# Performance work log

Hardware: AMD Instinct MI355X
Metric: run time of the kernel (lower is better)

Reference implementation:

```python
import jax, jax.numpy as jnp
import numpy as np

# MLA config (matches init_kwargs)
D = 2048
D_PRE_HEAD = 128
HEAD_NUM = 16
D_ROPE = D_PRE_HEAD // 2          # 64
DC_V = D_PRE_HEAD                 # 128
DC_KV = 4 * D_PRE_HEAD            # 512
DC_Q = 3 * DC_KV                  # 1536
Q_HEAD_DIM = D_PRE_HEAD + D_ROPE  # 192
MEG_D = D_PRE_HEAD + DC_V         # 256
MAX_LEN = 8192
EPS = 1e-7
BATCH, SEQ = 2, 2048


def rms_norm(x, w):
    x32 = x.astype(jnp.float32)
    var = jnp.mean(x32 * x32, axis=-1, keepdims=True)
    return w * (x32 * jax.lax.rsqrt(var + EPS)).astype(x.dtype)


def rope_reshape(x):
    # de-interleave pairs: [x0,x1,x2,x3,...] -> [x0,x2,...,x1,x3,...]
    b, h, s, d = x.shape
    return x.reshape(b, h, s, d // 2, 2).swapaxes(-1, -2).reshape(b, h, s, d)


def rope_rotate(x):
    half = x.shape[-1] // 2
    return jnp.concatenate([-x[..., half:], x[..., :half]], axis=-1)


def rope_tables(dtype=jnp.float32):
    inv_freq = 1.0 / (10000.0 ** (jnp.arange(0, D_ROPE, 2, dtype=jnp.float32) / D_ROPE))
    t = jnp.arange(MAX_LEN, dtype=jnp.float32)
    freqs = jnp.outer(t, inv_freq)                 # [MAX_LEN, D_ROPE/2]
    emb = jnp.concatenate([freqs, freqs], axis=-1)  # [MAX_LEN, D_ROPE]
    return jnp.cos(emb).astype(dtype), jnp.sin(emb).astype(dtype)


def setup_inputs() -> dict:
    key = jax.random.key(0)
    ks = jax.random.split(key, 8)
    s = 0.02
    x = jax.random.normal(ks[0], (BATCH, SEQ, D), dtype=jnp.float32)
    pos_ids = jnp.broadcast_to(jnp.arange(SEQ, dtype=jnp.int32)[None, :], (BATCH, SEQ))
    return {
        "x": x,
        "pos_ids": pos_ids,
        "w_q_down": jax.random.normal(ks[1], (DC_Q, D), dtype=jnp.float32) * s,
        "q_norm_w": jnp.ones((DC_Q,), dtype=jnp.float32),
        "w_q_up": jax.random.normal(ks[2], (HEAD_NUM * Q_HEAD_DIM, DC_Q), dtype=jnp.float32) * s,
        "w_kv_down": jax.random.normal(ks[3], (DC_KV + D_ROPE, D), dtype=jnp.float32) * s,
        "kv_norm_w": jnp.ones((DC_KV,), dtype=jnp.float32),
        "w_kv_up": jax.random.normal(ks[4], (HEAD_NUM * MEG_D, DC_KV), dtype=jnp.float32) * s,
        "w_out": jax.random.normal(ks[5], (D, HEAD_NUM * DC_V), dtype=jnp.float32) * s,
    }


def reference(x, pos_ids, w_q_down, q_norm_w, w_q_up, w_kv_down, kv_norm_w, w_kv_up, w_out):
    b, s, _ = x.shape
    # --- Q path: low-rank down -> norm -> up ---
    q = rms_norm(x @ w_q_down.T, q_norm_w) @ w_q_up.T          # [b,s,H*q_head_dim]
    q = q.reshape(b, s, HEAD_NUM, Q_HEAD_DIM).transpose(0, 2, 1, 3)  # [b,H,s,qhd]
    q_nope, q_rope = q[..., :D_PRE_HEAD], q[..., D_PRE_HEAD:]
    # --- KV path: shared compressed latent + decoupled rope key ---
    ckv_all = x @ w_kv_down.T                                   # [b,s,dc_kv+d_rope]
    c_kv, k_rope = ckv_all[..., :DC_KV], ckv_all[..., DC_KV:]
    c_kv = rms_norm(c_kv, kv_norm_w)
    kv = (c_kv @ w_kv_up.T).reshape(b, s, HEAD_NUM, MEG_D).transpose(0, 2, 1, 3)
    k_nope, value = kv[..., :D_PRE_HEAD], kv[..., D_PRE_HEAD:]  # [b,H,s,128] each
    k_rope = k_rope.reshape(b, s, 1, D_ROPE).transpose(0, 2, 1, 3)  # [b,1,s,64]
    # --- RoPE (decoupled path) ---
    cos, sin = rope_tables(x.dtype)
    cos_q = cos[pos_ids][:, None]   # [b,1,s,64]
    sin_q = sin[pos_ids][:, None]
    qr = rope_reshape(q_rope)
    kr = rope_reshape(k_rope)
    q_rope = qr * cos_q + rope_rotate(qr) * sin_q
    k_rope = kr * cos_q + rope_rotate(kr) * sin_q
    # --- attention ---
    query = jnp.concatenate([q_nope, q_rope], axis=-1)          # [b,H,s,192]
    key = jnp.concatenate(
        [k_nope, jnp.broadcast_to(k_rope, (b, HEAD_NUM, s, D_ROPE))], axis=-1)
    scale = 1.0 / jnp.sqrt(jnp.asarray(Q_HEAD_DIM, dtype=x.dtype))
    scores = jnp.einsum('bhqd,bhkd->bhqk', query, key) * scale
    causal = jnp.where(jnp.tril(jnp.ones((s, s), dtype=bool)), 0.0, -jnp.inf)
    scores = scores + causal[None, None].astype(scores.dtype)
    probs = jax.nn.softmax(scores, axis=-1)
    attn = jnp.einsum('bhqk,bhkd->bhqd', probs, value)          # [b,H,s,128]
    attn = attn.transpose(0, 2, 1, 3).reshape(b, s, HEAD_NUM * DC_V)
    return attn @ w_out.T
```

## Files before the change

### kernel.cpp

```cpp
#include <hip/hip_runtime.h>
#include <hip/hip_bf16.h>
#include <math.h>


#define T_TOK   4096
#define SEQ_LEN 2048
#define NB      2
#define NHEAD   16
#define DMODEL  2048
#define DCQ     1536
#define DCKV    512
#define DROPE   64
#define QHD     192
#define MEGD    256

typedef unsigned short u16;
typedef unsigned int   u32;
typedef __attribute__((ext_vector_type(8))) short short8v;
typedef __attribute__((ext_vector_type(4))) float f32x4;

__device__ __forceinline__ u16 f2bf(float f) {
    u32 u = __float_as_uint(f);
    u32 r = u + 0x7FFFu + ((u >> 16) & 1u);
    return (u16)(r >> 16);
}
__device__ __forceinline__ float bf2f(u16 h) {
    return __uint_as_float(((u32)h) << 16);
}

__global__ __launch_bounds__(256) void gemm_split_nt(
    const float* __restrict__ A, int lda,
    const float* __restrict__ W, int ldw,
    float* __restrict__ C, int ldc, int K)
{
    __shared__ __align__(16) u16 Ahs[64][32];
    __shared__ __align__(16) u16 Als[64][32];
    __shared__ __align__(16) u16 Whs[64][32];
    __shared__ __align__(16) u16 Wls[64][32];

    const int tid  = threadIdx.x;
    const int wave = tid >> 6;
    const int lane = tid & 63;
    const int wr = (wave >> 1) * 32;
    const int wc = (wave & 1) * 32;
    const int m0 = blockIdx.y * 64;
    const int n0 = blockIdx.x * 64;

    const int srow = tid >> 2;
    const int scol = (tid & 3) * 8;

    f32x4 acc[2][2];
    #pragma unroll
    for (int i = 0; i < 2; ++i)
        #pragma unroll
        for (int j = 0; j < 2; ++j)
            acc[i][j] = (f32x4){0.f, 0.f, 0.f, 0.f};

    const float* Ap = A + (size_t)(m0 + srow) * lda + scol;
    const float* Wp = W + (size_t)(n0 + srow) * ldw + scol;

    const int fr = lane & 15;
    const int kg = (lane >> 4) * 8;

    for (int k0 = 0; k0 < K; k0 += 32) {
        float av[8], wv[8];
        *(float4*)&av[0] = *(const float4*)(Ap + k0);
        *(float4*)&av[4] = *(const float4*)(Ap + k0 + 4);
        *(float4*)&wv[0] = *(const float4*)(Wp + k0);
        *(float4*)&wv[4] = *(const float4*)(Wp + k0 + 4);
        short8v ah, al, wh, wl;
        #pragma unroll
        for (int j = 0; j < 8; ++j) {
            u16 hb = f2bf(av[j]);
            ah[j] = (short)hb;
            al[j] = (short)f2bf(av[j] - bf2f(hb));
            u16 hw = f2bf(wv[j]);
            wh[j] = (short)hw;
            wl[j] = (short)f2bf(wv[j] - bf2f(hw));
        }
        __syncthreads();
        *(short8v*)&Ahs[srow][scol] = ah;
        *(short8v*)&Als[srow][scol] = al;
        *(short8v*)&Whs[srow][scol] = wh;
        *(short8v*)&Wls[srow][scol] = wl;
        __syncthreads();

        short8v afh[2], afl[2], wfh[2], wfl[2];
        #pragma unroll
        for (int i = 0; i < 2; ++i) {
            afh[i] = *(const short8v*)&Ahs[wr + i * 16 + fr][kg];
            afl[i] = *(const short8v*)&Als[wr + i * 16 + fr][kg];
            wfh[i] = *(const short8v*)&Whs[wc + i * 16 + fr][kg];
            wfl[i] = *(const short8v*)&Wls[wc + i * 16 + fr][kg];
        }
        #pragma unroll
        for (int i = 0; i < 2; ++i)
            #pragma unroll
            for (int j = 0; j < 2; ++j) {
                acc[i][j] = __builtin_amdgcn_mfma_f32_16x16x32_bf16(afh[i], wfh[j], acc[i][j], 0, 0, 0);
                acc[i][j] = __builtin_amdgcn_mfma_f32_16x16x32_bf16(afh[i], wfl[j], acc[i][j], 0, 0, 0);
                acc[i][j] = __builtin_amdgcn_mfma_f32_16x16x32_bf16(afl[i], wfh[j], acc[i][j], 0, 0, 0);
            }
    }

    const int rq = (lane >> 4) * 4;
    #pragma unroll
    for (int i = 0; i < 2; ++i)
        #pragma unroll
        for (int j = 0; j < 2; ++j)
            #pragma unroll
            for (int r = 0; r < 4; ++r)
                C[(size_t)(m0 + wr + i * 16 + rq + r) * ldc + (n0 + wc + j * 16 + fr)]
                    = acc[i][j][r];
}

template <int NPT>
__global__ __launch_bounds__(256) void rmsnorm_kernel(
    float* __restrict__ data, int stride, const float* __restrict__ w, int width)
{
    const int row = blockIdx.x;
    float* p = data + (size_t)row * stride;
    const int tid = threadIdx.x;

    float v[NPT];
    float ss = 0.f;
    #pragma unroll
    for (int i = 0; i < NPT; ++i) { v[i] = p[tid + i * 256]; ss += v[i] * v[i]; }
    #pragma unroll
    for (int off = 32; off; off >>= 1) ss += __shfl_xor(ss, off, 64);

    __shared__ float red[4];
    if ((tid & 63) == 0) red[tid >> 6] = ss;
    __syncthreads();
    ss = red[0] + red[1] + red[2] + red[3];

    const float scale = rsqrtf(ss / (float)width + 1e-7f);
    #pragma unroll
    for (int i = 0; i < NPT; ++i)
        p[tid + i * 256] = w[tid + i * 256] * (v[i] * scale);
}

__device__ __forceinline__ void rope_row(const float* __restrict__ vin,
                                         float* __restrict__ vout, float p)
{
    float buf[64];
    #pragma unroll
    for (int j = 0; j < 64; ++j) buf[j] = vin[j];
    #pragma unroll
    for (int j = 0; j < 32; ++j) {
        float f = powf(10000.f, -(float)j * (1.f / 32.f));
        float a = p * f;
        float c = cosf(a), s = sinf(a);
        vout[j]      = buf[2 * j] * c - buf[2 * j + 1] * s;
        vout[32 + j] = buf[2 * j + 1] * c + buf[2 * j] * s;
    }
}

__global__ __launch_bounds__(256) void rope_q_kernel(float* __restrict__ q,
                                                     const int* __restrict__ pos)
{
    const int idx = blockIdx.x * 256 + threadIdx.x;
    if (idx >= T_TOK * NHEAD) return;
    const int t = idx >> 4, h = idx & 15;
    float* v = q + (size_t)t * (NHEAD * QHD) + h * QHD + 128;
    rope_row(v, v, (float)pos[t]);
}

__global__ __launch_bounds__(256) void rope_k_kernel(const float* __restrict__ ckv,
                                                     const int* __restrict__ pos,
                                                     float* __restrict__ kr)
{
    const int t = blockIdx.x * 256 + threadIdx.x;
    if (t >= T_TOK) return;
    rope_row(ckv + (size_t)t * (DCKV + DROPE) + DCKV, kr + (size_t)t * DROPE,
             (float)pos[t]);
}

#define BQA   64
#define BKA   32
#define KSTR2 200
#define VSTR2 40
#define PSTR2 40

__global__ __launch_bounds__(256) void mla_attn_mfma(
    const float* __restrict__ q,
    const float* __restrict__ kv,
    const float* __restrict__ kr,
    float* __restrict__ o)
{
    __shared__ __align__(16) u16 KhS[BKA][KSTR2];
    __shared__ __align__(16) u16 KlS[BKA][KSTR2];
    __shared__ __align__(16) u16 VhS[128][VSTR2];
    __shared__ __align__(16) u16 VlS[128][VSTR2];
    __shared__ __align__(16) u16 PhS[4][16][PSTR2];
    __shared__ __align__(16) u16 PlS[4][16][PSTR2];

    const int qt = (int)(gridDim.x - 1) - (int)blockIdx.x;
    const int h  = blockIdx.y;
    const int b  = blockIdx.z;
    const int q0 = qt * BQA;
    const int tid  = threadIdx.x;
    const int wave = tid >> 6;
    const int lane = tid & 63;
    const int fr = lane & 15;
    const int gp = lane >> 4;
    const int kg = gp * 8;

    short8v qh[6], ql[6];
    {
        const float* qrow = q + (size_t)(b * SEQ_LEN + q0 + wave * 16 + fr) * (NHEAD * QHD)
                              + h * QHD;
        #pragma unroll
        for (int ks = 0; ks < 6; ++ks) {
            float v8[8];
            *(float4*)&v8[0] = *(const float4*)(qrow + ks * 32 + kg);
            *(float4*)&v8[4] = *(const float4*)(qrow + ks * 32 + kg + 4);
            #pragma unroll
            for (int j = 0; j < 8; ++j) {
                u16 hb = f2bf(v8[j]);
                qh[ks][j] = (short)hb;
                ql[ks][j] = (short)f2bf(v8[j] - bf2f(hb));
            }
        }
    }

    f32x4 acc_o[8];
    #pragma unroll
    for (int i = 0; i < 8; ++i) acc_o[i] = (f32x4){0.f, 0.f, 0.f, 0.f};
    float mrow[4] = {-1e30f, -1e30f, -1e30f, -1e30f};
    float lrow[4] = {0.f, 0.f, 0.f, 0.f};

    const float scale = 0.07216878364870323f;
    const int ntile = 2 * qt + 2;
    const int qmax_w = q0 + 16 * wave + 15;

    for (int kt = 0; kt < ntile; ++kt) {
        const int k0 = kt * BKA;
        __syncthreads();

        {
            const int krow = tid >> 3;
            const int c0 = (tid & 7) * 24;
            const int tk = b * SEQ_LEN + k0 + krow;
            float v24[24];
            #pragma unroll
            for (int i = 0; i < 6; ++i) {
                const int d = c0 + i * 4;
                float4 vv = (d < 128)
                    ? *(const float4*)(kv + (size_t)tk * (NHEAD * MEGD) + h * MEGD + d)
                    : *(const float4*)(kr + (size_t)tk * DROPE + (d - 128));
                *(float4*)&v24[i * 4] = vv;
            }
            #pragma unroll
            for (int i = 0; i < 6; ++i) {
                ushort4 hh, ll;
                u16* hp = &hh.x; u16* lp = &ll.x;
                #pragma unroll
                for (int j = 0; j < 4; ++j) {
                    float f = v24[i * 4 + j];
                    u16 hb = f2bf(f);
                    hp[j] = hb;
                    lp[j] = f2bf(f - bf2f(hb));
                }
                *(ushort4*)&KhS[krow][c0 + i * 4] = hh;
                *(ushort4*)&KlS[krow][c0 + i * 4] = ll;
            }
        }
        {
            const int kq = (tid & 7) * 4;
            const int dq = (tid >> 3) * 4;
            float4 vv[4];
            #pragma unroll
            for (int r = 0; r < 4; ++r) {
                const int tk = b * SEQ_LEN + k0 + kq + r;
                vv[r] = *(const float4*)(kv + (size_t)tk * (NHEAD * MEGD) + h * MEGD + 128 + dq);
            }
            const float* vp = (const float*)&vv[0];
            #pragma unroll
            for (int i = 0; i < 4; ++i) {
                ushort4 hh, ll;
                u16* hp = &hh.x; u16* lp = &ll.x;
                #pragma unroll
                for (int r = 0; r < 4; ++r) {
                    float f = vp[r * 4 + i];
                    u16 hb = f2bf(f);
                    hp[r] = hb;
                    lp[r] = f2bf(f - bf2f(hb));
                }
                *(ushort4*)&VhS[dq + i][kq] = hh;
                *(ushort4*)&VlS[dq + i][kq] = ll;
            }
        }
        __syncthreads();

        if (k0 <= qmax_w) {
            f32x4 s0 = (f32x4){0.f, 0.f, 0.f, 0.f};
            f32x4 s1 = (f32x4){0.f, 0.f, 0.f, 0.f};
            #pragma unroll
            for (int ks = 0; ks < 6; ++ks) {
                short8v kh0 = *(const short8v*)&KhS[fr][ks * 32 + kg];
                short8v kl0 = *(const short8v*)&KlS[fr][ks * 32 + kg];
                short8v kh1 = *(const short8v*)&KhS[fr + 16][ks * 32 + kg];
                short8v kl1 = *(const short8v*)&KlS[fr + 16][ks * 32 + kg];
                s0 = __builtin_amdgcn_mfma_f32_16x16x32_bf16(qh[ks], kh0, s0, 0, 0, 0);
                s0 = __builtin_amdgcn_mfma_f32_16x16x32_bf16(qh[ks], kl0, s0, 0, 0, 0);
                s0 = __builtin_amdgcn_mfma_f32_16x16x32_bf16(ql[ks], kh0, s0, 0, 0, 0);
                s1 = __builtin_amdgcn_mfma_f32_16x16x32_bf16(qh[ks], kh1, s1, 0, 0, 0);
                s1 = __builtin_amdgcn_mfma_f32_16x16x32_bf16(qh[ks], kl1, s1, 0, 0, 0);
                s1 = __builtin_amdgcn_mfma_f32_16x16x32_bf16(ql[ks], kh1, s1, 0, 0, 0);
            }
            float alpha[4];
            #pragma unroll
            for (int r = 0; r < 4; ++r) {
                const int qglob = q0 + wave * 16 + 4 * gp + r;
                float sc0 = (k0 + fr      <= qglob) ? s0[r] * scale : -1e30f;
                float sc1 = (k0 + 16 + fr <= qglob) ? s1[r] * scale : -1e30f;
                float mt = fmaxf(sc0, sc1);
                mt = fmaxf(mt, __shfl_xor(mt, 1, 64));
                mt = fmaxf(mt, __shfl_xor(mt, 2, 64));
                mt = fmaxf(mt, __shfl_xor(mt, 4, 64));
                mt = fmaxf(mt, __shfl_xor(mt, 8, 64));
                const float mnew = fmaxf(mrow[r], mt);
                alpha[r] = __expf(mrow[r] - mnew);
                const float p0 = __expf(sc0 - mnew);
                const float p1 = __expf(sc1 - mnew);
                float ps = p0 + p1;
                ps += __shfl_xor(ps, 1, 64);
                ps += __shfl_xor(ps, 2, 64);
                ps += __shfl_xor(ps, 4, 64);
                ps += __shfl_xor(ps, 8, 64);
                lrow[r] = lrow[r] * alpha[r] + ps;
                mrow[r] = mnew;
                u16 h0 = f2bf(p0);
                PhS[wave][4 * gp + r][fr]      = h0;
                PlS[wave][4 * gp + r][fr]      = f2bf(p0 - bf2f(h0));
                u16 h1 = f2bf(p1);
                PhS[wave][4 * gp + r][fr + 16] = h1;
                PlS[wave][4 * gp + r][fr + 16] = f2bf(p1 - bf2f(h1));
            }
            #pragma unroll
            for (int f2 = 0; f2 < 8; ++f2)
                #pragma unroll
                for (int r = 0; r < 4; ++r)
                    acc_o[f2][r] *= alpha[r];
            short8v ph = *(const short8v*)&PhS[wave][fr][kg];
            short8v pl = *(const short8v*)&PlS[wave][fr][kg];
            #pragma unroll
            for (int f2 = 0; f2 < 8; ++f2) {
                short8v vh = *(const short8v*)&VhS[fr + 16 * f2][kg];
                short8v vl = *(const short8v*)&VlS[fr + 16 * f2][kg];
                acc_o[f2] = __builtin_amdgcn_mfma_f32_16x16x32_bf16(ph, vh, acc_o[f2], 0, 0, 0);
                acc_o[f2] = __builtin_amdgcn_mfma_f32_16x16x32_bf16(ph, vl, acc_o[f2], 0, 0, 0);
                acc_o[f2] = __builtin_amdgcn_mfma_f32_16x16x32_bf16(pl, vh, acc_o[f2], 0, 0, 0);
            }
        }
    }

    float inv[4];
    #pragma unroll
    for (int r = 0; r < 4; ++r) inv[r] = 1.f / lrow[r];
    #pragma unroll
    for (int r = 0; r < 4; ++r) {
        const size_t t = (size_t)(b * SEQ_LEN + q0 + wave * 16 + 4 * gp + r);
        float* dst = o + t * (NHEAD * 128) + h * 128 + fr;
        #pragma unroll
        for (int f2 = 0; f2 < 8; ++f2)
            dst[16 * f2] = acc_o[f2][r] * inv[r];
    }
}

extern "C" void kernel_launch(void* const* d_in, const int* in_sizes, int n_in,
                              void* d_out, int out_size, void* d_ws, size_t ws_size,
                              hipStream_t stream)
{
    const float* x         = (const float*)d_in[0];
    const int*   pos       = (const int*)d_in[1];
    const float* w_q_down  = (const float*)d_in[2];
    const float* q_norm_w  = (const float*)d_in[3];
    const float* w_q_up    = (const float*)d_in[4];
    const float* w_kv_down = (const float*)d_in[5];
    const float* kv_norm_w = (const float*)d_in[6];
    const float* w_kv_up   = (const float*)d_in[7];
    const float* w_out     = (const float*)d_in[8];
    float* out = (float*)d_out;

    float* ws = (float*)d_ws;
    float* ao   = ws;
    float* q_dn = ws;
    float* ckv  = ws + (size_t)T_TOK * 2048;
    float* q_up = ckv + (size_t)T_TOK * (DCKV + DROPE);
    float* kvb  = q_up + (size_t)T_TOK * (NHEAD * QHD);
    float* kr   = kvb + (size_t)T_TOK * (NHEAD * MEGD);

    dim3 blk(256);
    gemm_split_nt<<<dim3(DCQ / 64, T_TOK / 64), blk, 0, stream>>>(
        x, DMODEL, w_q_down, DMODEL, q_dn, DCQ, DMODEL);
    gemm_split_nt<<<dim3((DCKV + DROPE) / 64, T_TOK / 64), blk, 0, stream>>>(
        x, DMODEL, w_kv_down, DMODEL, ckv, DCKV + DROPE, DMODEL);
    rmsnorm_kernel<6><<<T_TOK, 256, 0, stream>>>(q_dn, DCQ, q_norm_w, DCQ);
    rmsnorm_kernel<2><<<T_TOK, 256, 0, stream>>>(ckv, DCKV + DROPE, kv_norm_w, DCKV);
    rope_k_kernel<<<T_TOK / 256, 256, 0, stream>>>(ckv, pos, kr);
    gemm_split_nt<<<dim3((NHEAD * QHD) / 64, T_TOK / 64), blk, 0, stream>>>(
        q_dn, DCQ, w_q_up, DCQ, q_up, NHEAD * QHD, DCQ);
    gemm_split_nt<<<dim3((NHEAD * MEGD) / 64, T_TOK / 64), blk, 0, stream>>>(
        ckv, DCKV + DROPE, w_kv_up, DCKV, kvb, NHEAD * MEGD, DCKV);
    rope_q_kernel<<<(T_TOK * NHEAD) / 256, 256, 0, stream>>>(q_up, pos);
    mla_attn_mfma<<<dim3(SEQ_LEN / BQA, NHEAD, NB), dim3(256), 0, stream>>>(
        q_up, kvb, kr, ao);
    gemm_split_nt<<<dim3(DMODEL / 64, T_TOK / 64), blk, 0, stream>>>(
        ao, DMODEL, w_out, DMODEL, out, DMODEL, DMODEL);
}
```

Before: 1.400 ms.

## Enlarge split-bf16 GEMM tiles to 128x128, swizzle attention LDS, precompute RoPE frequencies

```diff
diff --git a/kernel.cpp b/kernel.cpp
--- a/kernel.cpp
+++ b/kernel.cpp
@@ -28,90 +28,99 @@
     return __uint_as_float(((u32)h) << 16);
 }
 
+#define GSTR 40
+
 __global__ __launch_bounds__(256) void gemm_split_nt(
     const float* __restrict__ A, int lda,
     const float* __restrict__ W, int ldw,
-    float* __restrict__ C, int ldc, int K)
-{
-    __shared__ __align__(16) u16 Ahs[64][32];
-    __shared__ __align__(16) u16 Als[64][32];
-    __shared__ __align__(16) u16 Whs[64][32];
-    __shared__ __align__(16) u16 Wls[64][32];
+    float* __restrict__ C, int ldc, int K, int N)
+{
+    __shared__ __align__(16) u16 Ahs[128][GSTR];
+    __shared__ __align__(16) u16 Als[128][GSTR];
+    __shared__ __align__(16) u16 Whs[128][GSTR];
+    __shared__ __align__(16) u16 Wls[128][GSTR];
 
     const int tid  = threadIdx.x;
     const int wave = tid >> 6;
     const int lane = tid & 63;
-    const int wr = (wave >> 1) * 32;
-    const int wc = (wave & 1) * 32;
-    const int m0 = blockIdx.y * 64;
-    const int n0 = blockIdx.x * 64;
-
-    const int srow = tid >> 2;
-    const int scol = (tid & 3) * 8;
-
-    f32x4 acc[2][2];
-    #pragma unroll
-    for (int i = 0; i < 2; ++i)
-        #pragma unroll
-        for (int j = 0; j < 2; ++j)
-            acc[i][j] = (f32x4){0.f, 0.f, 0.f, 0.f};
-
-    const float* Ap = A + (size_t)(m0 + srow) * lda + scol;
-    const float* Wp = W + (size_t)(n0 + srow) * ldw + scol;
-
+    const int wr = (wave >> 1) * 64;
+    const int wc = (wave & 1) * 64;
+    const int m0 = blockIdx.y * 128;
+    const int n0 = blockIdx.x * 128;
     const int fr = lane & 15;
     const int kg = (lane >> 4) * 8;
 
+    f32x4 acc[4][4];
+    #pragma unroll
+    for (int i = 0; i < 4; ++i)
+        #pragma unroll
+        for (int j = 0; j < 4; ++j)
+            acc[i][j] = (f32x4){0.f, 0.f, 0.f, 0.f};
+
+    const int r0 = tid >> 2,          c0 = (tid & 3) * 8;
+    const int r1 = (tid + 256) >> 2,  c1 = c0;
+    const int an0 = m0 + r0, an1 = m0 + r1;
+    const int wn0 = (n0 + r0 < N) ? n0 + r0 : N - 1;
+    const int wn1 = (n0 + r1 < N) ? n0 + r1 : N - 1;
+
     for (int k0 = 0; k0 < K; k0 += 32) {
-        float av[8], wv[8];
-        *(float4*)&av[0] = *(const float4*)(Ap + k0);
-        *(float4*)&av[4] = *(const float4*)(Ap + k0 + 4);
-        *(float4*)&wv[0] = *(const float4*)(Wp + k0);
-        *(float4*)&wv[4] = *(const float4*)(Wp + k0 + 4);
-        short8v ah, al, wh, wl;
+        float a0[8], a1[8], w0[8], w1[8];
+        *(float4*)&a0[0] = *(const float4*)(A + (size_t)an0 * lda + k0 + c0);
+        *(float4*)&a0[4] = *(const float4*)(A + (size_t)an0 * lda + k0 + c0 + 4);
+        *(float4*)&a1[0] = *(const float4*)(A + (size_t)an1 * lda + k0 + c1);
+        *(float4*)&a1[4] = *(const float4*)(A + (size_t)an1 * lda + k0 + c1 + 4);
+        *(float4*)&w0[0] = *(const float4*)(W + (size_t)wn0 * ldw + k0 + c0);
+        *(float4*)&w0[4] = *(const float4*)(W + (size_t)wn0 * ldw + k0 + c0 + 4);
+        *(float4*)&w1[0] = *(const float4*)(W + (size_t)wn1 * ldw + k0 + c1);
+        *(float4*)&w1[4] = *(const float4*)(W + (size_t)wn1 * ldw + k0 + c1 + 4);
+
+        short8v a0h, a0l, a1h, a1l, w0h, w0l, w1h, w1l;
         #pragma unroll
         for (int j = 0; j < 8; ++j) {
-            u16 hb = f2bf(av[j]);
-            ah[j] = (short)hb;
-            al[j] = (short)f2bf(av[j] - bf2f(hb));
-            u16 hw = f2bf(wv[j]);
-            wh[j] = (short)hw;
-            wl[j] = (short)f2bf(wv[j] - bf2f(hw));
+            u16 hb;
+            hb = f2bf(a0[j]); a0h[j] = (short)hb; a0l[j] = (short)f2bf(a0[j] - bf2f(hb));
+            hb = f2bf(a1[j]); a1h[j] = (short)hb; a1l[j] = (short)f2bf(a1[j] - bf2f(hb));
+            hb = f2bf(w0[j]); w0h[j] = (short)hb; w0l[j] = (short)f2bf(w0[j] - bf2f(hb));
+            hb = f2bf(w1[j]); w1h[j] = (short)hb; w1l[j] = (short)f2bf(w1[j] - bf2f(hb));
         }
         __syncthreads();
-        *(short8v*)&Ahs[srow][scol] = ah;
-        *(short8v*)&Als[srow][scol] = al;
-        *(short8v*)&Whs[srow][scol] = wh;
-        *(short8v*)&Wls[srow][scol] = wl;
+        *(short8v*)&Ahs[r0][c0] = a0h;  *(short8v*)&Als[r0][c0] = a0l;
+        *(short8v*)&Ahs[r1][c1] = a1h;  *(short8v*)&Als[r1][c1] = a1l;
+        *(short8v*)&Whs[r0][c0] = w0h;  *(short8v*)&Wls[r0][c0] = w0l;
+        *(short8v*)&Whs[r1][c1] = w1h;  *(short8v*)&Wls[r1][c1] = w1l;
         __syncthreads();
 
-        short8v afh[2], afl[2], wfh[2], wfl[2];
-        #pragma unroll
-        for (int i = 0; i < 2; ++i) {
-            afh[i] = *(const short8v*)&Ahs[wr + i * 16 + fr][kg];
-            afl[i] = *(const short8v*)&Als[wr + i * 16 + fr][kg];
-            wfh[i] = *(const short8v*)&Whs[wc + i * 16 + fr][kg];
-            wfl[i] = *(const short8v*)&Wls[wc + i * 16 + fr][kg];
-        }
-        #pragma unroll
-        for (int i = 0; i < 2; ++i)
-            #pragma unroll
-            for (int j = 0; j < 2; ++j) {
-                acc[i][j] = __builtin_amdgcn_mfma_f32_16x16x32_bf16(afh[i], wfh[j], acc[i][j], 0, 0, 0);
-                acc[i][j] = __builtin_amdgcn_mfma_f32_16x16x32_bf16(afh[i], wfl[j], acc[i][j], 0, 0, 0);
-                acc[i][j] = __builtin_amdgcn_mfma_f32_16x16x32_bf16(afl[i], wfh[j], acc[i][j], 0, 0, 0);
-            }
+        short8v wfh[4], wfl[4];
+        #pragma unroll
+        for (int nj = 0; nj < 4; ++nj) {
+            wfh[nj] = *(const short8v*)&Whs[wc + nj * 16 + fr][kg];
+            wfl[nj] = *(const short8v*)&Wls[wc + nj * 16 + fr][kg];
+        }
+        #pragma unroll
+        for (int mi = 0; mi < 4; ++mi) {
+            short8v ah = *(const short8v*)&Ahs[wr + mi * 16 + fr][kg];
+            short8v al = *(const short8v*)&Als[wr + mi * 16 + fr][kg];
+            #pragma unroll
+            for (int nj = 0; nj < 4; ++nj) {
+                acc[mi][nj] = __builtin_amdgcn_mfma_f32_16x16x32_bf16(ah, wfh[nj], acc[mi][nj], 0, 0, 0);
+                acc[mi][nj] = __builtin_amdgcn_mfma_f32_16x16x32_bf16(ah, wfl[nj], acc[mi][nj], 0, 0, 0);
+                acc[mi][nj] = __builtin_amdgcn_mfma_f32_16x16x32_bf16(al, wfh[nj], acc[mi][nj], 0, 0, 0);
+            }
+        }
     }
 
     const int rq = (lane >> 4) * 4;
     #pragma unroll
-    for (int i = 0; i < 2; ++i)
-        #pragma unroll
-        for (int j = 0; j < 2; ++j)
-            #pragma unroll
-            for (int r = 0; r < 4; ++r)
-                C[(size_t)(m0 + wr + i * 16 + rq + r) * ldc + (n0 + wc + j * 16 + fr)]
-                    = acc[i][j][r];
+    for (int mi = 0; mi < 4; ++mi)
+        #pragma unroll
+        for (int nj = 0; nj < 4; ++nj) {
+            const int col = n0 + wc + nj * 16 + fr;
+            if (col < N) {
+                #pragma unroll
+                for (int r = 0; r < 4; ++r)
+                    C[(size_t)(m0 + wr + mi * 16 + rq + r) * ldc + col] = acc[mi][nj][r];
+            }
+        }
 }
 
 template <int NPT>
@@ -141,15 +150,15 @@
 }
 
 __device__ __forceinline__ void rope_row(const float* __restrict__ vin,
-                                         float* __restrict__ vout, float p)
+                                         float* __restrict__ vout, float p,
+                                         const float* __restrict__ ftab)
 {
     float buf[64];
     #pragma unroll
     for (int j = 0; j < 64; ++j) buf[j] = vin[j];
     #pragma unroll
     for (int j = 0; j < 32; ++j) {
-        float f = powf(10000.f, -(float)j * (1.f / 32.f));
-        float a = p * f;
+        float a = p * ftab[j];
         float c = cosf(a), s = sinf(a);
         vout[j]      = buf[2 * j] * c - buf[2 * j + 1] * s;
         vout[32 + j] = buf[2 * j + 1] * c + buf[2 * j] * s;
@@ -159,28 +168,37 @@
 __global__ __launch_bounds__(256) void rope_q_kernel(float* __restrict__ q,
                                                      const int* __restrict__ pos)
 {
+    __shared__ float ftab[32];
+    if (threadIdx.x < 32)
+        ftab[threadIdx.x] = powf(10000.f, -(float)threadIdx.x * (1.f / 32.f));
+    __syncthreads();
     const int idx = blockIdx.x * 256 + threadIdx.x;
     if (idx >= T_TOK * NHEAD) return;
     const int t = idx >> 4, h = idx & 15;
     float* v = q + (size_t)t * (NHEAD * QHD) + h * QHD + 128;
-    rope_row(v, v, (float)pos[t]);
+    rope_row(v, v, (float)pos[t], ftab);
 }
 
 __global__ __launch_bounds__(256) void rope_k_kernel(const float* __restrict__ ckv,
                                                      const int* __restrict__ pos,
                                                      float* __restrict__ kr)
 {
+    __shared__ float ftab[32];
+    if (threadIdx.x < 32)
+        ftab[threadIdx.x] = powf(10000.f, -(float)threadIdx.x * (1.f / 32.f));
+    __syncthreads();
     const int t = blockIdx.x * 256 + threadIdx.x;
     if (t >= T_TOK) return;
     rope_row(ckv + (size_t)t * (DCKV + DROPE) + DCKV, kr + (size_t)t * DROPE,
-             (float)pos[t]);
+             (float)pos[t], ftab);
 }
 
 #define BQA   64
 #define BKA   32
-#define KSTR2 200
-#define VSTR2 40
 #define PSTR2 40
+
+#define KSWZ(row, colu16) ((((row) * 192 + (colu16)) * 2) ^ (((row) & 7) << 4))
+#define VSWZ(row, colu16) ((((row) * 32 + (colu16)) * 2) ^ (((row) & 7) << 4))
 
 __global__ __launch_bounds__(256) void mla_attn_mfma(
     const float* __restrict__ q,
@@ -188,10 +206,10 @@
     const float* __restrict__ kr,
     float* __restrict__ o)
 {
-    __shared__ __align__(16) u16 KhS[BKA][KSTR2];
-    __shared__ __align__(16) u16 KlS[BKA][KSTR2];
-    __shared__ __align__(16) u16 VhS[128][VSTR2];
-    __shared__ __align__(16) u16 VlS[128][VSTR2];
+    __shared__ __align__(128) u16 KhS[32 * 192];
+    __shared__ __align__(128) u16 KlS[32 * 192];
+    __shared__ __align__(128) u16 VhS[128 * 32];
+    __shared__ __align__(128) u16 VlS[128 * 32];
     __shared__ __align__(16) u16 PhS[4][16][PSTR2];
     __shared__ __align__(16) u16 PlS[4][16][PSTR2];
 
@@ -206,6 +224,11 @@
     const int gp = lane >> 4;
     const int kg = gp * 8;
 
+    char* KhB = (char*)&KhS[0];
+    char* KlB = (char*)&KlS[0];
+    char* VhB = (char*)&VhS[0];
+    char* VlB = (char*)&VlS[0];
+
     short8v qh[6], ql[6];
     {
         const float* qrow = q + (size_t)(b * SEQ_LEN + q0 + wave * 16 + fr) * (NHEAD * QHD)
@@ -238,33 +261,32 @@
         const int k0 = kt * BKA;
         __syncthreads();
 
-        {
-            const int krow = tid >> 3;
-            const int c0 = (tid & 7) * 24;
+        #pragma unroll
+        for (int i = 0; i < 3; ++i) {
+            const int s = tid + 256 * i;
+            const int krow = s / 24;
+            const int c = (s % 24) * 8;
             const int tk = b * SEQ_LEN + k0 + krow;
-            float v24[24];
-            #pragma unroll
-            for (int i = 0; i < 6; ++i) {
-                const int d = c0 + i * 4;
-                float4 vv = (d < 128)
-                    ? *(const float4*)(kv + (size_t)tk * (NHEAD * MEGD) + h * MEGD + d)
-                    : *(const float4*)(kr + (size_t)tk * DROPE + (d - 128));
-                *(float4*)&v24[i * 4] = vv;
-            }
-            #pragma unroll
-            for (int i = 0; i < 6; ++i) {
-                ushort4 hh, ll;
-                u16* hp = &hh.x; u16* lp = &ll.x;
-                #pragma unroll
-                for (int j = 0; j < 4; ++j) {
-                    float f = v24[i * 4 + j];
-                    u16 hb = f2bf(f);
-                    hp[j] = hb;
-                    lp[j] = f2bf(f - bf2f(hb));
-                }
-                *(ushort4*)&KhS[krow][c0 + i * 4] = hh;
-                *(ushort4*)&KlS[krow][c0 + i * 4] = ll;
-            }
+            float v8[8];
+            if (c < 128) {
+                const float* src = kv + (size_t)tk * (NHEAD * MEGD) + h * MEGD + c;
+                *(float4*)&v8[0] = *(const float4*)(src);
+                *(float4*)&v8[4] = *(const float4*)(src + 4);
+            } else {
+                const float* src = kr + (size_t)tk * DROPE + (c - 128);
+                *(float4*)&v8[0] = *(const float4*)(src);
+                *(float4*)&v8[4] = *(const float4*)(src + 4);
+            }
+            short8v hh, ll;
+            #pragma unroll
+            for (int j = 0; j < 8; ++j) {
+                u16 hb = f2bf(v8[j]);
+                hh[j] = (short)hb;
+                ll[j] = (short)f2bf(v8[j] - bf2f(hb));
+            }
+            const int bo = KSWZ(krow, c);
+            *(short8v*)(KhB + bo) = hh;
+            *(short8v*)(KlB + bo) = ll;
         }
         {
             const int kq = (tid & 7) * 4;
@@ -287,8 +309,9 @@
                     hp[r] = hb;
                     lp[r] = f2bf(f - bf2f(hb));
                 }
-                *(ushort4*)&VhS[dq + i][kq] = hh;
-                *(ushort4*)&VlS[dq + i][kq] = ll;
+                const int bo = VSWZ(dq + i, kq);
+                *(ushort4*)(VhB + bo) = hh;
+                *(ushort4*)(VlB + bo) = ll;
             }
         }
         __syncthreads();
@@ -298,10 +321,12 @@
             f32x4 s1 = (f32x4){0.f, 0.f, 0.f, 0.f};
             #pragma unroll
             for (int ks = 0; ks < 6; ++ks) {
-                short8v kh0 = *(const short8v*)&KhS[fr][ks * 32 + kg];
-                short8v kl0 = *(const short8v*)&KlS[fr][ks * 32 + kg];
-                short8v kh1 = *(const short8v*)&KhS[fr + 16][ks * 32 + kg];
-                short8v kl1 = *(const short8v*)&KlS[fr + 16][ks * 32 + kg];
+                const int b0 = KSWZ(fr,      ks * 32 + kg);
+                const int b1 = KSWZ(fr + 16, ks * 32 + kg);
+                short8v kh0 = *(const short8v*)(KhB + b0);
+                short8v kl0 = *(const short8v*)(KlB + b0);
+                short8v kh1 = *(const short8v*)(KhB + b1);
+                short8v kl1 = *(const short8v*)(KlB + b1);
                 s0 = __builtin_amdgcn_mfma_f32_16x16x32_bf16(qh[ks], kh0, s0, 0, 0, 0);
                 s0 = __builtin_amdgcn_mfma_f32_16x16x32_bf16(qh[ks], kl0, s0, 0, 0, 0);
                 s0 = __builtin_amdgcn_mfma_f32_16x16x32_bf16(ql[ks], kh0, s0, 0, 0, 0);
@@ -347,8 +372,9 @@
             short8v pl = *(const short8v*)&PlS[wave][fr][kg];
             #pragma unroll
             for (int f2 = 0; f2 < 8; ++f2) {
-                short8v vh = *(const short8v*)&VhS[fr + 16 * f2][kg];
-                short8v vl = *(const short8v*)&VlS[fr + 16 * f2][kg];
+                const int bo = VSWZ(fr + 16 * f2, kg);
+                short8v vh = *(const short8v*)(VhB + bo);
+                short8v vl = *(const short8v*)(VlB + bo);
                 acc_o[f2] = __builtin_amdgcn_mfma_f32_16x16x32_bf16(ph, vh, acc_o[f2], 0, 0, 0);
                 acc_o[f2] = __builtin_amdgcn_mfma_f32_16x16x32_bf16(ph, vl, acc_o[f2], 0, 0, 0);
                 acc_o[f2] = __builtin_amdgcn_mfma_f32_16x16x32_bf16(pl, vh, acc_o[f2], 0, 0, 0);
@@ -393,20 +419,20 @@
     float* kr   = kvb + (size_t)T_TOK * (NHEAD * MEGD);
 
     dim3 blk(256);
-    gemm_split_nt<<<dim3(DCQ / 64, T_TOK / 64), blk, 0, stream>>>(
-        x, DMODEL, w_q_down, DMODEL, q_dn, DCQ, DMODEL);
-    gemm_split_nt<<<dim3((DCKV + DROPE) / 64, T_TOK / 64), blk, 0, stream>>>(
-        x, DMODEL, w_kv_down, DMODEL, ckv, DCKV + DROPE, DMODEL);
+    gemm_split_nt<<<dim3(DCQ / 128, T_TOK / 128), blk, 0, stream>>>(
+        x, DMODEL, w_q_down, DMODEL, q_dn, DCQ, DMODEL, DCQ);
+    gemm_split_nt<<<dim3((DCKV + DROPE + 127) / 128, T_TOK / 128), blk, 0, stream>>>(
+        x, DMODEL, w_kv_down, DMODEL, ckv, DCKV + DROPE, DMODEL, DCKV + DROPE);
     rmsnorm_kernel<6><<<T_TOK, 256, 0, stream>>>(q_dn, DCQ, q_norm_w, DCQ);
     rmsnorm_kernel<2><<<T_TOK, 256, 0, stream>>>(ckv, DCKV + DROPE, kv_norm_w, DCKV);
     rope_k_kernel<<<T_TOK / 256, 256, 0, stream>>>(ckv, pos, kr);
-    gemm_split_nt<<<dim3((NHEAD * QHD) / 64, T_TOK / 64), blk, 0, stream>>>(
-        q_dn, DCQ, w_q_up, DCQ, q_up, NHEAD * QHD, DCQ);
-    gemm_split_nt<<<dim3((NHEAD * MEGD) / 64, T_TOK / 64), blk, 0, stream>>>(
-        ckv, DCKV + DROPE, w_kv_up, DCKV, kvb, NHEAD * MEGD, DCKV);
+    gemm_split_nt<<<dim3((NHEAD * QHD) / 128, T_TOK / 128), blk, 0, stream>>>(
+        q_dn, DCQ, w_q_up, DCQ, q_up, NHEAD * QHD, DCQ, NHEAD * QHD);
+    gemm_split_nt<<<dim3((NHEAD * MEGD) / 128, T_TOK / 128), blk, 0, stream>>>(
+        ckv, DCKV + DROPE, w_kv_up, DCKV, kvb, NHEAD * MEGD, DCKV, NHEAD * MEGD);
     rope_q_kernel<<<(T_TOK * NHEAD) / 256, 256, 0, stream>>>(q_up, pos);
     mla_attn_mfma<<<dim3(SEQ_LEN / BQA, NHEAD, NB), dim3(256), 0, stream>>>(
         q_up, kvb, kr, ao);
-    gemm_split_nt<<<dim3(DMODEL / 64, T_TOK / 64), blk, 0, stream>>>(
-        ao, DMODEL, w_out, DMODEL, out, DMODEL, DMODEL);
-}
+    gemm_split_nt<<<dim3(DMODEL / 128, T_TOK / 128), blk, 0, stream>>>(
+        ao, DMODEL, w_out, DMODEL, out, DMODEL, DMODEL, DMODEL);
+}
```

Result: slower. 1.684 ms (+20.3%).
